# Kernel tuning notes

Measured on AMD Instinct MI355X. Metric: run time of the kernel, lower is better.

## Reference

```python
import jax, jax.numpy as jnp
import numpy as np

B, T, DIM = 1, 2048, 4096
N_HEADS, N_KV_HEADS, HEAD_DIM = 32, 8, 128
N_REP = N_HEADS // N_KV_HEADS
ROPE_THETA = 10000.0


def setup_inputs() -> dict:
    key = jax.random.key(0)
    ks = jax.random.split(key, 6)
    # rotary angle tables: [T, head_dim//2]
    inv_freq = 1.0 / (ROPE_THETA ** (np.arange(0, HEAD_DIM, 2, dtype=np.float32) / HEAD_DIM))
    angles = np.arange(T, dtype=np.float32)[:, None] * inv_freq[None, :]
    scale = 0.02
    return {
        "x": jax.random.normal(ks[0], (B, T, DIM), dtype=jnp.float32),
        "rope_cos": jnp.asarray(np.cos(angles)),
        "rope_sin": jnp.asarray(np.sin(angles)),
        "wq": jax.random.normal(ks[1], (DIM, N_HEADS * HEAD_DIM), dtype=jnp.float32) * scale,
        "wk": jax.random.normal(ks[2], (DIM, N_KV_HEADS * HEAD_DIM), dtype=jnp.float32) * scale,
        "wv": jax.random.normal(ks[3], (DIM, N_KV_HEADS * HEAD_DIM), dtype=jnp.float32) * scale,
        "wo": jax.random.normal(ks[4], (N_HEADS * HEAD_DIM, DIM), dtype=jnp.float32) * scale,
    }


def _apply_rope(x, cos, sin):
    # x: [B, T, H, D]; cos/sin: [T, D//2] -- complex multiply on (even, odd) pairs
    xr = x.astype(jnp.float32).reshape(*x.shape[:-1], -1, 2)
    a, b = xr[..., 0], xr[..., 1]
    c = cos[None, : x.shape[1], None, :]
    s = sin[None, : x.shape[1], None, :]
    rot = jnp.stack([a * c - b * s, a * s + b * c], axis=-1)
    return rot.reshape(x.shape).astype(x.dtype)


def reference(x, rope_cos, rope_sin, wq, wk, wv, wo):
    Bq, Tq, _ = x.shape
    q = (x @ wq).reshape(Bq, Tq, N_HEADS, HEAD_DIM)
    k = (x @ wk).reshape(Bq, Tq, N_KV_HEADS, HEAD_DIM)
    v = (x @ wv).reshape(Bq, Tq, N_KV_HEADS, HEAD_DIM)
    q = _apply_rope(q, rope_cos, rope_sin)
    k = _apply_rope(k, rope_cos, rope_sin)
    # GQA: group query heads with their shared KV head instead of materializing repeated K/V
    qg = q.reshape(Bq, Tq, N_KV_HEADS, N_REP, HEAD_DIM)
    scale = 1.0 / jnp.sqrt(jnp.asarray(HEAD_DIM, dtype=q.dtype))
    scores = jnp.einsum("bqgrd,bkgd->bgrqk", qg, k) * scale  # [B,G,R,T,T]
    causal = jnp.tril(jnp.ones((Tq, Tq), dtype=bool))
    scores = jnp.where(causal[None, None, None], scores, jnp.finfo(scores.dtype).min)
    attn = jax.nn.softmax(scores, axis=-1)
    ctx = jnp.einsum("bgrqk,bkgd->bqgrd", attn, v).reshape(Bq, Tq, N_HEADS * HEAD_DIM)
    return ctx @ wo
```

## Files before the change

### kernel.cpp

```cpp
#include <hip/hip_runtime.h>
#include <hip/hip_bf16.h>

#define T_SEQ 2048
#define DIM 4096
#define NH 32
#define NKV 8
#define HD 128
#define QKV_N 6144

typedef __bf16 bf16x8 __attribute__((ext_vector_type(8)));
typedef float f32x4 __attribute__((ext_vector_type(4)));

__device__ __forceinline__ void storev(float* p, float v) { *p = v; }
__device__ __forceinline__ void storev(__hip_bfloat16* p, float v) { *p = __float2bfloat16(v); }

__device__ __forceinline__ void gl_lds16(const __hip_bfloat16* g, __hip_bfloat16* l) {
    __builtin_amdgcn_global_load_lds(
        (const __attribute__((address_space(1))) unsigned int*)g,
        (__attribute__((address_space(3))) unsigned int*)l, 16, 0, 0);
}

__global__ void cast_x(const float* __restrict__ in, __hip_bfloat16* __restrict__ out, int n) {
    int i = (blockIdx.x * 256 + threadIdx.x) * 4;
    if (i < n) {
        float4 v = *(const float4*)(in + i);
        out[i + 0] = __float2bfloat16(v.x);
        out[i + 1] = __float2bfloat16(v.y);
        out[i + 2] = __float2bfloat16(v.z);
        out[i + 3] = __float2bfloat16(v.w);
    }
}

__global__ void tcast(const float* __restrict__ in, __hip_bfloat16* __restrict__ out,
                      int R, int C, int out_stride, int row_off) {
    __shared__ float tile[32][33];
    int tx = threadIdx.x, ty = threadIdx.y;
    int r0 = blockIdx.y * 32, c0 = blockIdx.x * 32;
    for (int k = 0; k < 4; k++)
        tile[ty + 8 * k][tx] = in[(size_t)(r0 + ty + 8 * k) * C + c0 + tx];
    __syncthreads();
    for (int k = 0; k < 4; k++)
        out[(size_t)(c0 + ty + 8 * k + row_off) * out_stride + r0 + tx] =
            __float2bfloat16(tile[tx][ty + 8 * k]);
}

__global__ void vtrans(const __hip_bfloat16* __restrict__ qkv, __hip_bfloat16* __restrict__ vt) {
    __shared__ __hip_bfloat16 tile[32][33];
    int tx = threadIdx.x, ty = threadIdx.y;
    int t0 = blockIdx.x * 32, d0 = blockIdx.y * 32, g = blockIdx.z;
    for (int k = 0; k < 4; k++)
        tile[ty + 8 * k][tx] = qkv[(size_t)(t0 + ty + 8 * k) * QKV_N + 5120 + g * HD + d0 + tx];
    __syncthreads();
    for (int k = 0; k < 4; k++)
        vt[(size_t)g * HD * T_SEQ + (size_t)(d0 + ty + 8 * k) * T_SEQ + t0 + tx] =
            tile[tx][ty + 8 * k];
}

__global__ void rope_kernel(__hip_bfloat16* qkv, const float* __restrict__ cosb,
                            const float* __restrict__ sinb) {
    int idx = blockIdx.x * 256 + threadIdx.x;
    int t = idx / 2560;
    int rem = idx % 2560;
    int hs = rem >> 6, i = rem & 63;
    int col = hs < 32 ? hs * HD + 2 * i : DIM + (hs - 32) * HD + 2 * i;
    size_t base = (size_t)t * QKV_N + col;
    float a = __bfloat162float(qkv[base]);
    float b = __bfloat162float(qkv[base + 1]);
    float c = cosb[t * 64 + i], s = sinb[t * 64 + i];
    qkv[base]     = __float2bfloat16(a * c - b * s);
    qkv[base + 1] = __float2bfloat16(a * s + b * c);
}

template <typename OutT>
__global__ __launch_bounds__(256, 2) void gemm_bt(const __hip_bfloat16* __restrict__ A,
                                                  const __hip_bfloat16* __restrict__ Bt,
                                                  OutT* __restrict__ C, int M, int N, int K) {
    __shared__ __hip_bfloat16 sA[128 * 32];
    __shared__ __hip_bfloat16 sB[128 * 32];
    int tid = threadIdx.x;
    int wave = tid >> 6, lane = tid & 63, quad = lane >> 4, l15 = lane & 15;
    int wm = wave >> 1, wn = wave & 1;
    int m0 = blockIdx.y * 128, n0 = blockIdx.x * 128;
    f32x4 acc[4][4] = {};
    for (int k0 = 0; k0 < K; k0 += 32) {
        __syncthreads();
        for (int r = 0; r < 2; r++) {
            int seg = tid + 256 * r;
            int row = seg >> 2, col = (seg & 3) * 8;
            gl_lds16(&A[(size_t)(m0 + row) * K + k0 + col], &sA[row * 32 + col]);
            gl_lds16(&Bt[(size_t)(n0 + row) * K + k0 + col], &sB[row * 32 + col]);
        }
        __syncthreads();
        bf16x8 af[4], bfr[4];
        for (int i = 0; i < 4; i++)
            af[i] = *(const bf16x8*)&sA[(wm * 64 + i * 16 + l15) * 32 + quad * 8];
        for (int j = 0; j < 4; j++)
            bfr[j] = *(const bf16x8*)&sB[(wn * 64 + j * 16 + l15) * 32 + quad * 8];
        for (int i = 0; i < 4; i++)
            for (int j = 0; j < 4; j++)
                acc[i][j] = __builtin_amdgcn_mfma_f32_16x16x32_bf16(af[i], bfr[j], acc[i][j], 0, 0, 0);
    }
    for (int i = 0; i < 4; i++)
        for (int j = 0; j < 4; j++)
            for (int r = 0; r < 4; r++) {
                int row = m0 + wm * 64 + i * 16 + quad * 4 + r;
                int col = n0 + wn * 64 + j * 16 + l15;
                storev(&C[(size_t)row * N + col], acc[i][j][r]);
            }
}

__global__ __launch_bounds__(256, 2) void attn_kernel(const __hip_bfloat16* __restrict__ qkv,
                                                      const __hip_bfloat16* __restrict__ vt,
                                                      __hip_bfloat16* __restrict__ ctx) {
    __shared__ __align__(16) __hip_bfloat16 sk[64][136];
    __shared__ __align__(16) __hip_bfloat16 sv[128][72];
    __shared__ __align__(16) __hip_bfloat16 sp[4][16][72];
    int tid = threadIdx.x;
    int wave = tid >> 6, lane = tid & 63, quad = lane >> 4, l15 = lane & 15;
    int pair = blockIdx.x, h = blockIdx.y, g = h >> 2;
    const float scale = 0.08838834764831845f;

    for (int rep = 0; rep < 2; rep++) {
        int qb = rep ? (31 - pair) : pair;
        int q0 = qb * 64 + wave * 16;

        bf16x8 qf[4];
        for (int ks = 0; ks < 4; ks++)
            qf[ks] = *(const bf16x8*)&qkv[(size_t)(q0 + l15) * QKV_N + h * HD + ks * 32 + quad * 8];

        f32x4 o[8] = {};
        float m_r[4], l_r[4];
        for (int r = 0; r < 4; r++) { m_r[r] = -1e30f; l_r[r] = 0.f; }
        int nkt = qb + 1;

        for (int kt = 0; kt < nkt; kt++) {
            __syncthreads();
            for (int rr = 0; rr < 4; rr++) {
                int seg = tid + 256 * rr;
                {
                    int row = seg >> 4, col = (seg & 15) * 8;
                    *(uint4*)&sk[row][col] =
                        *(const uint4*)&qkv[(size_t)(kt * 64 + row) * QKV_N + DIM + g * HD + col];
                }
                {
                    int row = seg >> 3, col = (seg & 7) * 8;
                    *(uint4*)&sv[row][col] =
                        *(const uint4*)&vt[(size_t)g * HD * T_SEQ + (size_t)row * T_SEQ + kt * 64 + col];
                }
            }
            __syncthreads();
            f32x4 s[4] = {};
            for (int ks = 0; ks < 4; ks++)
                for (int n = 0; n < 4; n++) {
                    bf16x8 kf = *(const bf16x8*)&sk[n * 16 + l15][ks * 32 + quad * 8];
                    s[n] = __builtin_amdgcn_mfma_f32_16x16x32_bf16(qf[ks], kf, s[n], 0, 0, 0);
                }
            bool diag = (kt == qb);
            float alpha[4];
            for (int r = 0; r < 4; r++) {
                float v0 = s[0][r] * scale, v1 = s[1][r] * scale;
                float v2 = s[2][r] * scale, v3 = s[3][r] * scale;
                if (diag) {
                    int qrow = q0 + quad * 4 + r;
                    int k0i = kt * 64 + l15;
                    if (k0i      > qrow) v0 = -1e30f;
                    if (k0i + 16 > qrow) v1 = -1e30f;
                    if (k0i + 32 > qrow) v2 = -1e30f;
                    if (k0i + 48 > qrow) v3 = -1e30f;
                }
                float mx = fmaxf(fmaxf(v0, v1), fmaxf(v2, v3));
                for (int off = 1; off < 16; off <<= 1) mx = fmaxf(mx, __shfl_xor(mx, off));
                float mn = fmaxf(m_r[r], mx);
                float al = __expf(m_r[r] - mn);
                m_r[r] = mn;
                float e0 = __expf(v0 - mn), e1 = __expf(v1 - mn);
                float e2 = __expf(v2 - mn), e3 = __expf(v3 - mn);
                float rs = e0 + e1 + e2 + e3;
                for (int off = 1; off < 16; off <<= 1) rs += __shfl_xor(rs, off);
                l_r[r] = l_r[r] * al + rs;
                alpha[r] = al;
                int qr = quad * 4 + r;
                sp[wave][qr][l15]      = __float2bfloat16(e0);
                sp[wave][qr][16 + l15] = __float2bfloat16(e1);
                sp[wave][qr][32 + l15] = __float2bfloat16(e2);
                sp[wave][qr][48 + l15] = __float2bfloat16(e3);
            }
            for (int j = 0; j < 8; j++)
                for (int r = 0; r < 4; r++) o[j][r] *= alpha[r];
            asm volatile("s_waitcnt lgkmcnt(0)" ::: "memory");
            bf16x8 pf0 = *(const bf16x8*)&sp[wave][l15][quad * 8];
            bf16x8 pf1 = *(const bf16x8*)&sp[wave][l15][32 + quad * 8];
            for (int j = 0; j < 8; j++) {
                bf16x8 vf0 = *(const bf16x8*)&sv[j * 16 + l15][quad * 8];
                bf16x8 vf1 = *(const bf16x8*)&sv[j * 16 + l15][32 + quad * 8];
                o[j] = __builtin_amdgcn_mfma_f32_16x16x32_bf16(pf0, vf0, o[j], 0, 0, 0);
                o[j] = __builtin_amdgcn_mfma_f32_16x16x32_bf16(pf1, vf1, o[j], 0, 0, 0);
            }
        }
        float rl[4];
        for (int r = 0; r < 4; r++) rl[r] = 1.f / l_r[r];
        for (int j = 0; j < 8; j++)
            for (int r = 0; r < 4; r++) {
                int row = q0 + quad * 4 + r;
                int col = h * HD + j * 16 + l15;
                ctx[(size_t)row * DIM + col] = __float2bfloat16(o[j][r] * rl[r]);
            }
    }
}

extern "C" void kernel_launch(void* const* d_in, const int* in_sizes, int n_in,
                              void* d_out, int out_size, void* d_ws, size_t ws_size,
                              hipStream_t stream) {
    const float* x        = (const float*)d_in[0];
    const float* rope_cos = (const float*)d_in[1];
    const float* rope_sin = (const float*)d_in[2];
    const float* wq       = (const float*)d_in[3];
    const float* wk       = (const float*)d_in[4];
    const float* wv       = (const float*)d_in[5];
    const float* wo       = (const float*)d_in[6];
    float* out = (float*)d_out;

    char* ws = (char*)d_ws;
    size_t need = 0;
    need += (size_t)T_SEQ * DIM * 2;
    need += (size_t)QKV_N * DIM * 2;
    need += (size_t)DIM * DIM * 2;
    need += (size_t)T_SEQ * QKV_N * 2;
    need += (size_t)NKV * HD * T_SEQ * 2;
    need += (size_t)T_SEQ * DIM * 2;
    if (ws_size < need) return;

    __hip_bfloat16* x_bf   = (__hip_bfloat16*)ws; ws += (size_t)T_SEQ * DIM * 2;
    __hip_bfloat16* wqkv_t = (__hip_bfloat16*)ws; ws += (size_t)QKV_N * DIM * 2;
    __hip_bfloat16* wo_t   = (__hip_bfloat16*)ws; ws += (size_t)DIM * DIM * 2;
    __hip_bfloat16* qkv    = (__hip_bfloat16*)ws; ws += (size_t)T_SEQ * QKV_N * 2;
    __hip_bfloat16* vt     = (__hip_bfloat16*)ws; ws += (size_t)NKV * HD * T_SEQ * 2;
    __hip_bfloat16* ctx    = (__hip_bfloat16*)ws; ws += (size_t)T_SEQ * DIM * 2;

    dim3 tb(32, 8);
    cast_x<<<8192, 256, 0, stream>>>(x, x_bf, T_SEQ * DIM);
    tcast<<<dim3(128, 128), tb, 0, stream>>>(wq, wqkv_t, DIM, 4096, 4096, 0);
    tcast<<<dim3(32, 128), tb, 0, stream>>>(wk, wqkv_t, DIM, 1024, 4096, 4096);
    tcast<<<dim3(32, 128), tb, 0, stream>>>(wv, wqkv_t, DIM, 1024, 4096, 5120);
    tcast<<<dim3(128, 128), tb, 0, stream>>>(wo, wo_t, DIM, 4096, 4096, 0);

    gemm_bt<__hip_bfloat16><<<dim3(48, 16), 256, 0, stream>>>(x_bf, wqkv_t, qkv, T_SEQ, QKV_N, DIM);
    rope_kernel<<<20480, 256, 0, stream>>>(qkv, rope_cos, rope_sin);
    vtrans<<<dim3(64, 4, 8), tb, 0, stream>>>(qkv, vt);
    attn_kernel<<<dim3(16, 32), 256, 0, stream>>>(qkv, vt, ctx);
    gemm_bt<float><<<dim3(32, 16), 256, 0, stream>>>(ctx, wo_t, out, T_SEQ, DIM, DIM);
}
```

Measured before the change: 539.4 us.

## Vectorize weight transpose-cast and RoPE, double K-step per GEMM barrier

The weight transpose-cast kernel moves to 64x64 tiles with float4 loads and 16-byte bf16 stores, and RoPE processes 8 bf16 values per thread using vector loads of cos/sin. The GEMM stages 64 K elements per iteration into two LDS sub-buffers, which halves the number of barrier pairs. All three aim to cut memory-instruction and synchronization overhead, at the cost of more LDS per GEMM block and larger per-thread register use.

New measurement: 503.4 us. -6.7%, faster.

```diff
diff --git a/kernel.cpp b/kernel.cpp
--- a/kernel.cpp
+++ b/kernel.cpp
@@ -13,6 +13,11 @@
 
 __device__ __forceinline__ void storev(float* p, float v) { *p = v; }
 __device__ __forceinline__ void storev(__hip_bfloat16* p, float v) { *p = __float2bfloat16(v); }
+
+__device__ __forceinline__ float bf2f(unsigned short u) {
+    unsigned int t = ((unsigned int)u) << 16;
+    return __builtin_bit_cast(float, t);
+}
 
 __device__ __forceinline__ void gl_lds16(const __hip_bfloat16* g, __hip_bfloat16* l) {
     __builtin_amdgcn_global_load_lds(
@@ -33,15 +38,27 @@
 
 __global__ void tcast(const float* __restrict__ in, __hip_bfloat16* __restrict__ out,
                       int R, int C, int out_stride, int row_off) {
-    __shared__ float tile[32][33];
-    int tx = threadIdx.x, ty = threadIdx.y;
-    int r0 = blockIdx.y * 32, c0 = blockIdx.x * 32;
-    for (int k = 0; k < 4; k++)
-        tile[ty + 8 * k][tx] = in[(size_t)(r0 + ty + 8 * k) * C + c0 + tx];
+    __shared__ float tile[64][65];
+    int tid = threadIdx.x;
+    int r0 = blockIdx.y * 64, c0 = blockIdx.x * 64;
+    for (int it = 0; it < 4; it++) {
+        int row = (tid >> 4) + 16 * it;
+        int c4 = (tid & 15) * 4;
+        float4 v = *(const float4*)&in[(size_t)(r0 + row) * C + c0 + c4];
+        tile[row][c4 + 0] = v.x;
+        tile[row][c4 + 1] = v.y;
+        tile[row][c4 + 2] = v.z;
+        tile[row][c4 + 3] = v.w;
+    }
     __syncthreads();
-    for (int k = 0; k < 4; k++)
-        out[(size_t)(c0 + ty + 8 * k + row_off) * out_stride + r0 + tx] =
-            __float2bfloat16(tile[tx][ty + 8 * k]);
+    for (int it = 0; it < 2; it++) {
+        int orow = (tid >> 3) + 32 * it;
+        int oc8 = (tid & 7) * 8;
+        __hip_bfloat16 tmp[8];
+        for (int j = 0; j < 8; j++)
+            tmp[j] = __float2bfloat16(tile[oc8 + j][orow]);
+        *(uint4*)&out[(size_t)(c0 + orow + row_off) * out_stride + r0 + oc8] = *(uint4*)tmp;
+    }
 }
 
 __global__ void vtrans(const __hip_bfloat16* __restrict__ qkv, __hip_bfloat16* __restrict__ vt) {
@@ -59,46 +76,56 @@
 __global__ void rope_kernel(__hip_bfloat16* qkv, const float* __restrict__ cosb,
                             const float* __restrict__ sinb) {
     int idx = blockIdx.x * 256 + threadIdx.x;
-    int t = idx / 2560;
-    int rem = idx % 2560;
-    int hs = rem >> 6, i = rem & 63;
-    int col = hs < 32 ? hs * HD + 2 * i : DIM + (hs - 32) * HD + 2 * i;
+    int t = idx / 640;
+    int col = (idx % 640) * 8;
+    int i0 = (col & 127) >> 1;
     size_t base = (size_t)t * QKV_N + col;
-    float a = __bfloat162float(qkv[base]);
-    float b = __bfloat162float(qkv[base + 1]);
-    float c = cosb[t * 64 + i], s = sinb[t * 64 + i];
-    qkv[base]     = __float2bfloat16(a * c - b * s);
-    qkv[base + 1] = __float2bfloat16(a * s + b * c);
+    unsigned short u[8];
+    *(uint4*)u = *(const uint4*)&qkv[base];
+    float4 cv = *(const float4*)&cosb[t * 64 + i0];
+    float4 sv = *(const float4*)&sinb[t * 64 + i0];
+    float c[4] = {cv.x, cv.y, cv.z, cv.w}, s[4] = {sv.x, sv.y, sv.z, sv.w};
+    __hip_bfloat16 o[8];
+    for (int j = 0; j < 4; j++) {
+        float a = bf2f(u[2 * j]), b = bf2f(u[2 * j + 1]);
+        o[2 * j]     = __float2bfloat16(a * c[j] - b * s[j]);
+        o[2 * j + 1] = __float2bfloat16(a * s[j] + b * c[j]);
+    }
+    *(uint4*)&qkv[base] = *(uint4*)o;
 }
 
 template <typename OutT>
 __global__ __launch_bounds__(256, 2) void gemm_bt(const __hip_bfloat16* __restrict__ A,
                                                   const __hip_bfloat16* __restrict__ Bt,
                                                   OutT* __restrict__ C, int M, int N, int K) {
-    __shared__ __hip_bfloat16 sA[128 * 32];
-    __shared__ __hip_bfloat16 sB[128 * 32];
+    __shared__ __hip_bfloat16 sA[2][128 * 32];
+    __shared__ __hip_bfloat16 sB[2][128 * 32];
     int tid = threadIdx.x;
     int wave = tid >> 6, lane = tid & 63, quad = lane >> 4, l15 = lane & 15;
     int wm = wave >> 1, wn = wave & 1;
     int m0 = blockIdx.y * 128, n0 = blockIdx.x * 128;
     f32x4 acc[4][4] = {};
-    for (int k0 = 0; k0 < K; k0 += 32) {
+    for (int k0 = 0; k0 < K; k0 += 64) {
         __syncthreads();
         for (int r = 0; r < 2; r++) {
             int seg = tid + 256 * r;
             int row = seg >> 2, col = (seg & 3) * 8;
-            gl_lds16(&A[(size_t)(m0 + row) * K + k0 + col], &sA[row * 32 + col]);
-            gl_lds16(&Bt[(size_t)(n0 + row) * K + k0 + col], &sB[row * 32 + col]);
+            gl_lds16(&A[(size_t)(m0 + row) * K + k0 + col],       &sA[0][row * 32 + col]);
+            gl_lds16(&A[(size_t)(m0 + row) * K + k0 + 32 + col],  &sA[1][row * 32 + col]);
+            gl_lds16(&Bt[(size_t)(n0 + row) * K + k0 + col],      &sB[0][row * 32 + col]);
+            gl_lds16(&Bt[(size_t)(n0 + row) * K + k0 + 32 + col], &sB[1][row * 32 + col]);
         }
         __syncthreads();
-        bf16x8 af[4], bfr[4];
-        for (int i = 0; i < 4; i++)
-            af[i] = *(const bf16x8*)&sA[(wm * 64 + i * 16 + l15) * 32 + quad * 8];
-        for (int j = 0; j < 4; j++)
-            bfr[j] = *(const bf16x8*)&sB[(wn * 64 + j * 16 + l15) * 32 + quad * 8];
-        for (int i = 0; i < 4; i++)
+        for (int ks = 0; ks < 2; ks++) {
+            bf16x8 af[4], bfr[4];
+            for (int i = 0; i < 4; i++)
+                af[i] = *(const bf16x8*)&sA[ks][(wm * 64 + i * 16 + l15) * 32 + quad * 8];
             for (int j = 0; j < 4; j++)
-                acc[i][j] = __builtin_amdgcn_mfma_f32_16x16x32_bf16(af[i], bfr[j], acc[i][j], 0, 0, 0);
+                bfr[j] = *(const bf16x8*)&sB[ks][(wn * 64 + j * 16 + l15) * 32 + quad * 8];
+            for (int i = 0; i < 4; i++)
+                for (int j = 0; j < 4; j++)
+                    acc[i][j] = __builtin_amdgcn_mfma_f32_16x16x32_bf16(af[i], bfr[j], acc[i][j], 0, 0, 0);
+        }
     }
     for (int i = 0; i < 4; i++)
         for (int j = 0; j < 4; j++)
@@ -237,16 +264,15 @@
     __hip_bfloat16* vt     = (__hip_bfloat16*)ws; ws += (size_t)NKV * HD * T_SEQ * 2;
     __hip_bfloat16* ctx    = (__hip_bfloat16*)ws; ws += (size_t)T_SEQ * DIM * 2;
 
-    dim3 tb(32, 8);
     cast_x<<<8192, 256, 0, stream>>>(x, x_bf, T_SEQ * DIM);
-    tcast<<<dim3(128, 128), tb, 0, stream>>>(wq, wqkv_t, DIM, 4096, 4096, 0);
-    tcast<<<dim3(32, 128), tb, 0, stream>>>(wk, wqkv_t, DIM, 1024, 4096, 4096);
-    tcast<<<dim3(32, 128), tb, 0, stream>>>(wv, wqkv_t, DIM, 1024, 4096, 5120);
-    tcast<<<dim3(128, 128), tb, 0, stream>>>(wo, wo_t, DIM, 4096, 4096, 0);
+    tcast<<<dim3(64, 64), 256, 0, stream>>>(wq, wqkv_t, DIM, 4096, 4096, 0);
+    tcast<<<dim3(16, 64), 256, 0, stream>>>(wk, wqkv_t, DIM, 1024, 4096, 4096);
+    tcast<<<dim3(16, 64), 256, 0, stream>>>(wv, wqkv_t, DIM, 1024, 4096, 5120);
+    tcast<<<dim3(64, 64), 256, 0, stream>>>(wo, wo_t, DIM, 4096, 4096, 0);
 
     gemm_bt<__hip_bfloat16><<<dim3(48, 16), 256, 0, stream>>>(x_bf, wqkv_t, qkv, T_SEQ, QKV_N, DIM);
-    rope_kernel<<<20480, 256, 0, stream>>>(qkv, rope_cos, rope_sin);
-    vtrans<<<dim3(64, 4, 8), tb, 0, stream>>>(qkv, vt);
+    rope_kernel<<<5120, 256, 0, stream>>>(qkv, rope_cos, rope_sin);
+    vtrans<<<dim3(64, 4, 8), dim3(32, 8), 0, stream>>>(qkv, vt);
     attn_kernel<<<dim3(16, 32), 256, 0, stream>>>(qkv, vt, ctx);
     gemm_bt<float><<<dim3(32, 16), 256, 0, stream>>>(ctx, wo_t, out, T_SEQ, DIM, DIM);
 }
```
